# Kernel tuning notes

Hardware: AMD Instinct MI355X
Metric: run time of the kernel (lower is better)

The kernel has to match this reference:

```python
import jax, jax.numpy as jnp
import numpy as np

N_NODES = 100000
N_EDGES = 1000000
EMB_DIM = 64
N_LAYERS = 5
NUM_CLASS = 10
NUM_GRAPHS = 128
BN_EPS = 1e-5


def setup_inputs() -> dict:
    key = jax.random.key(0)
    ks = jax.random.split(key, 16)
    s = 0.05
    inp = {
        "x": jnp.zeros((N_NODES,), dtype=jnp.int64),
        "edge_index": jax.random.randint(ks[0], (2, N_EDGES), 0, N_NODES, dtype=jnp.int64),
        "edge_attr": jax.random.normal(ks[1], (N_EDGES, 7), dtype=jnp.float32),
        "batch": jnp.sort(jax.random.randint(ks[2], (N_NODES,), 0, NUM_GRAPHS, dtype=jnp.int64)),
        # parameters
        "node_table": jax.random.normal(ks[3], (1, EMB_DIM), dtype=jnp.float32) * s,
        "ew": jax.random.normal(ks[4], (N_LAYERS, 7, EMB_DIM), dtype=jnp.float32) * s,   # edge_encoder weight
        "eb": jax.random.normal(ks[5], (N_LAYERS, EMB_DIM), dtype=jnp.float32) * s,
        "w1": jax.random.normal(ks[6], (N_LAYERS, EMB_DIM, EMB_DIM), dtype=jnp.float32) * s,
        "b1": jax.random.normal(ks[7], (N_LAYERS, EMB_DIM), dtype=jnp.float32) * s,
        "w2": jax.random.normal(ks[8], (N_LAYERS, EMB_DIM, EMB_DIM), dtype=jnp.float32) * s,
        "b2": jax.random.normal(ks[9], (N_LAYERS, EMB_DIM), dtype=jnp.float32) * s,
        "gamma": jnp.ones((N_LAYERS, EMB_DIM), dtype=jnp.float32),
        "beta": jnp.zeros((N_LAYERS, EMB_DIM), dtype=jnp.float32),
        "pw": jax.random.normal(ks[10], (EMB_DIM, NUM_CLASS), dtype=jnp.float32) * s,
        "pb": jnp.zeros((NUM_CLASS,), dtype=jnp.float32),
    }
    return inp


def reference(x, edge_index, edge_attr, batch, node_table, ew, eb, w1, b1, w2, b2, gamma, beta, pw, pb):
    n = x.shape[0]
    src, dst = edge_index[0], edge_index[1]
    h = node_table[x]  # [N, D] node embedding lookup (all index 0)
    for l in range(N_LAYERS):
        edge_emb = edge_attr @ ew[l] + eb[l]                      # [E, D]
        msg = jax.nn.relu(h[src] + edge_emb)                      # gather + add + relu
        agg = jax.ops.segment_sum(msg, dst, num_segments=n)       # scatter-add
        z = h + agg                                               # (1 + eps)*x with eps=0
        z = jax.nn.relu(z @ w1[l] + b1[l]) @ w2[l] + b2[l]        # GIN MLP
        mu = z.mean(axis=0)
        var = z.var(axis=0)                                       # biased var, matches BN training
        z = (z - mu) * jax.lax.rsqrt(var + BN_EPS) * gamma[l] + beta[l]
        if l != N_LAYERS - 1:
            z = jax.nn.relu(z)                                    # dropout is identity (eval)
        h = z
    # global mean pool over graphs
    sums = jax.ops.segment_sum(h, batch, num_segments=NUM_GRAPHS)           # [B, D]
    cnt = jax.ops.segment_sum(jnp.ones((n,), h.dtype), batch, num_segments=NUM_GRAPHS)
    h_graph = sums / jnp.maximum(cnt, 1.0)[:, None]
    return h_graph @ pw + pb
```

## Files before the change

### kernel.cpp

```cpp
#include <hip/hip_runtime.h>


__global__ void hist_k(const int* __restrict__ dst, int* __restrict__ cnt, int E) {
  int stride = gridDim.x * blockDim.x;
  for (int i = blockIdx.x * blockDim.x + threadIdx.x; i < E; i += stride)
    atomicAdd(&cnt[dst[i]], 1);
}

__global__ void scan_a_k(const int* __restrict__ deg, int* __restrict__ rowptr,
                         int* __restrict__ bsum, int n) {
  __shared__ int s[256];
  int i = blockIdx.x * 256 + threadIdx.x;
  int v = (i < n) ? deg[i] : 0;
  s[threadIdx.x] = v;
  __syncthreads();
  for (int off = 1; off < 256; off <<= 1) {
    int t = (threadIdx.x >= off) ? s[threadIdx.x - off] : 0;
    __syncthreads();
    s[threadIdx.x] += t;
    __syncthreads();
  }
  if (i < n) rowptr[i] = s[threadIdx.x] - v;
  if (threadIdx.x == 255) bsum[blockIdx.x] = s[255];
}

__global__ void scan_b_k(int* __restrict__ bsum, int nb) {
  __shared__ int s[512];
  int t = threadIdx.x;
  int v = (t < nb) ? bsum[t] : 0;
  s[t] = v;
  __syncthreads();
  for (int off = 1; off < 512; off <<= 1) {
    int u = (t >= off) ? s[t - off] : 0;
    __syncthreads();
    s[t] += u;
    __syncthreads();
  }
  if (t < nb) bsum[t] = s[t] - v;
}

__global__ void scan_c_k(int* __restrict__ rowptr, int* __restrict__ cur,
                         const int* __restrict__ bsum, int n, int E) {
  int i = blockIdx.x * 256 + threadIdx.x;
  if (i < n) {
    int r = rowptr[i] + bsum[blockIdx.x];
    rowptr[i] = r;
    cur[i] = r;
  }
  if (i == 0) rowptr[n] = E;
}

__global__ void scatter_k(const int* __restrict__ src, const int* __restrict__ dst,
                          int* __restrict__ cur, float* __restrict__ sea,
                          const float* __restrict__ ea, int E) {
  int stride = gridDim.x * blockDim.x;
  for (int i = blockIdx.x * blockDim.x + threadIdx.x; i < E; i += stride) {
    int d = dst[i];
    int pos = atomicAdd(&cur[d], 1);
    const float* a = ea + (size_t)i * 7;
    float4 lo = make_float4(a[0], a[1], a[2], a[3]);
    float4 hi = make_float4(a[4], a[5], a[6], __int_as_float(src[i]));
    float4* o = (float4*)(sea + (size_t)pos * 8);
    o[0] = lo;
    o[1] = hi;
  }
}

#define NPW 8
template<int MODE>
__global__ __launch_bounds__(256)
void agg_k(const float* __restrict__ hprev, const int* __restrict__ x,
           const float* __restrict__ ntab, const int* __restrict__ rowptr,
           const float* __restrict__ sea, const float* __restrict__ ewl,
           const float* __restrict__ ebl, const float* __restrict__ statsP,
           const float* __restrict__ gamP, const float* __restrict__ betP,
           float* __restrict__ zout, int n) {
  int wv = (blockIdx.x * blockDim.x + threadIdx.x) >> 6;
  int lane = threadIdx.x & 63;
  int g0 = wv * NPW;
  if (g0 >= n) return;
  int gend = g0 + NPW; if (gend > n) gend = n;

  float ew_[7];
#pragma unroll
  for (int k = 0; k < 7; k++) ew_[k] = ewl[k * 64 + lane];
  float ebv = ebl[lane];

  float cnst = 0.f, sc = 1.f, sh = 0.f;
  if (MODE == 0) cnst = ntab[lane];
  if (MODE == 2) {
    float s1 = statsP[lane], s2 = statsP[64 + lane];
    float mu = s1 / (float)n;
    float var = s2 / (float)n - mu * mu;
    sc = gamP[lane] * rsqrtf(var + 1e-5f);
    sh = betP[lane] - mu * sc;
  }

  auto Hg = [&](int row) -> float {
    if (MODE == 1) {
      int xv = __builtin_amdgcn_readfirstlane(x[row]);
      return ntab[(size_t)xv * 64 + lane];
    } else {
      float v = hprev[(size_t)row * 64 + lane];
      return fmaxf(fmaf(v, sc, sh), 0.f);
    }
  };

  int pcur = __builtin_amdgcn_readfirstlane(rowptr[g0]);
  for (int nd = g0; nd < gend; nd++) {
    int pnext = __builtin_amdgcn_readfirstlane(rowptr[nd + 1]);
    float acc = (MODE == 0) ? cnst : Hg(nd);
    int p = pcur;
    for (; p + 4 <= pnext; p += 4) {
      const float* R0 = sea + (size_t)p * 8;
      const float* R1 = R0 + 8;
      const float* R2 = R0 + 16;
      const float* R3 = R0 + 24;
      float h0, h1, h2, h3;
      if (MODE != 0) {
        int s0 = __builtin_amdgcn_readfirstlane(__float_as_int(R0[7]));
        int s1 = __builtin_amdgcn_readfirstlane(__float_as_int(R1[7]));
        int s2 = __builtin_amdgcn_readfirstlane(__float_as_int(R2[7]));
        int s3 = __builtin_amdgcn_readfirstlane(__float_as_int(R3[7]));
        h0 = Hg(s0); h1 = Hg(s1); h2 = Hg(s2); h3 = Hg(s3);
      } else {
        h0 = h1 = h2 = h3 = cnst;
      }
      float m0 = ebv, m1 = ebv, m2 = ebv, m3 = ebv;
#pragma unroll
      for (int k = 0; k < 7; k++) {
        m0 = fmaf(R0[k], ew_[k], m0);
        m1 = fmaf(R1[k], ew_[k], m1);
        m2 = fmaf(R2[k], ew_[k], m2);
        m3 = fmaf(R3[k], ew_[k], m3);
      }
      acc += fmaxf(h0 + m0, 0.f);
      acc += fmaxf(h1 + m1, 0.f);
      acc += fmaxf(h2 + m2, 0.f);
      acc += fmaxf(h3 + m3, 0.f);
    }
    for (; p < pnext; p++) {
      const float* R0 = sea + (size_t)p * 8;
      float h0 = cnst;
      if (MODE != 0) {
        int s0 = __builtin_amdgcn_readfirstlane(__float_as_int(R0[7]));
        h0 = Hg(s0);
      }
      float m0 = ebv;
#pragma unroll
      for (int k = 0; k < 7; k++) m0 = fmaf(R0[k], ew_[k], m0);
      acc += fmaxf(h0 + m0, 0.f);
    }
    zout[(size_t)nd * 64 + lane] = acc;
    pcur = pnext;
  }
}

#define ASTR 132
__global__ __launch_bounds__(256, 3)
void mlp_k(const float* __restrict__ zin, const float* __restrict__ w1l,
           const float* __restrict__ b1l, const float* __restrict__ w2l,
           const float* __restrict__ b2l, float* __restrict__ zout,
           float* __restrict__ statslot, int n) {
  __shared__ float As[64 * ASTR];
  __shared__ float Ws[4096];
  __shared__ float red[128];
  int tid = threadIdx.x;
  int tx = tid & 15, ty = tid >> 4;
  if (tid < 128) red[tid] = 0.f;
  int r0 = blockIdx.x * 128;

  float4 w2r[4];
  {
    const float4* wb = (const float4*)w2l;
#pragma unroll
    for (int it = 0; it < 4; it++) w2r[it] = wb[it * 256 + tid];
  }

  {
    const float4* gz = (const float4*)(zin + (size_t)r0 * 64);
#pragma unroll
    for (int it = 0; it < 8; it++) {
      int f4 = it * 256 + tid;
      int row = f4 >> 4, kq = f4 & 15;
      float4 v = make_float4(0.f, 0.f, 0.f, 0.f);
      if (r0 + row < n) v = gz[f4];
      As[(4 * kq + 0) * ASTR + row] = v.x;
      As[(4 * kq + 1) * ASTR + row] = v.y;
      As[(4 * kq + 2) * ASTR + row] = v.z;
      As[(4 * kq + 3) * ASTR + row] = v.w;
    }
    const float4* wa = (const float4*)w1l;
    float4* wd = (float4*)Ws;
#pragma unroll
    for (int it = 0; it < 4; it++) wd[it * 256 + tid] = wa[it * 256 + tid];
  }
  __syncthreads();

  const float4 b1v = *(const float4*)(b1l + tx * 4);
  float t[8][4];
#pragma unroll
  for (int rr = 0; rr < 8; rr++) {
    t[rr][0] = b1v.x; t[rr][1] = b1v.y; t[rr][2] = b1v.z; t[rr][3] = b1v.w;
  }
#pragma unroll 8
  for (int k = 0; k < 64; k++) {
    float4 aA = *(const float4*)&As[k * ASTR + ty * 8];
    float4 aB = *(const float4*)&As[k * ASTR + ty * 8 + 4];
    float4 b = *(const float4*)&Ws[k * 64 + tx * 4];
    float a[8] = {aA.x, aA.y, aA.z, aA.w, aB.x, aB.y, aB.z, aB.w};
#pragma unroll
    for (int rr = 0; rr < 8; rr++) {
      t[rr][0] = fmaf(a[rr], b.x, t[rr][0]);
      t[rr][1] = fmaf(a[rr], b.y, t[rr][1]);
      t[rr][2] = fmaf(a[rr], b.z, t[rr][2]);
      t[rr][3] = fmaf(a[rr], b.w, t[rr][3]);
    }
  }
  __syncthreads();

#pragma unroll
  for (int cc = 0; cc < 4; cc++)
#pragma unroll
    for (int rr = 0; rr < 8; rr++)
      As[(tx * 4 + cc) * ASTR + ty * 8 + rr] = fmaxf(t[rr][cc], 0.f);
  {
    float4* wd = (float4*)Ws;
#pragma unroll
    for (int it = 0; it < 4; it++) wd[it * 256 + tid] = w2r[it];
  }
  __syncthreads();

  const float4 b2v = *(const float4*)(b2l + tx * 4);
  float o[8][4];
#pragma unroll
  for (int rr = 0; rr < 8; rr++) {
    o[rr][0] = b2v.x; o[rr][1] = b2v.y; o[rr][2] = b2v.z; o[rr][3] = b2v.w;
  }
#pragma unroll 8
  for (int k = 0; k < 64; k++) {
    float4 aA = *(const float4*)&As[k * ASTR + ty * 8];
    float4 aB = *(const float4*)&As[k * ASTR + ty * 8 + 4];
    float4 b = *(const float4*)&Ws[k * 64 + tx * 4];
    float a[8] = {aA.x, aA.y, aA.z, aA.w, aB.x, aB.y, aB.z, aB.w};
#pragma unroll
    for (int rr = 0; rr < 8; rr++) {
      o[rr][0] = fmaf(a[rr], b.x, o[rr][0]);
      o[rr][1] = fmaf(a[rr], b.y, o[rr][1]);
      o[rr][2] = fmaf(a[rr], b.z, o[rr][2]);
      o[rr][3] = fmaf(a[rr], b.w, o[rr][3]);
    }
  }

  float s1[4] = {0.f, 0.f, 0.f, 0.f}, s2[4] = {0.f, 0.f, 0.f, 0.f};
#pragma unroll
  for (int rr = 0; rr < 8; rr++) {
    int grow = r0 + ty * 8 + rr;
    if (grow < n) {
      float4 v = make_float4(o[rr][0], o[rr][1], o[rr][2], o[rr][3]);
      *(float4*)(zout + (size_t)grow * 64 + tx * 4) = v;
#pragma unroll
      for (int cc = 0; cc < 4; cc++) {
        s1[cc] += o[rr][cc];
        s2[cc] = fmaf(o[rr][cc], o[rr][cc], s2[cc]);
      }
    }
  }
#pragma unroll
  for (int cc = 0; cc < 4; cc++) {
    s1[cc] += __shfl_xor(s1[cc], 16); s1[cc] += __shfl_xor(s1[cc], 32);
    s2[cc] += __shfl_xor(s2[cc], 16); s2[cc] += __shfl_xor(s2[cc], 32);
  }
  if ((tid & 48) == 0) {
#pragma unroll
    for (int cc = 0; cc < 4; cc++) {
      atomicAdd(&red[tx * 4 + cc], s1[cc]);
      atomicAdd(&red[64 + tx * 4 + cc], s2[cc]);
    }
  }
  __syncthreads();
  if (tid < 128) atomicAdd(&statslot[tid], red[tid]);
}

__global__ void pool_k(const float* __restrict__ z2, const float* __restrict__ stats,
                       const float* __restrict__ gam, const float* __restrict__ bet,
                       const int* __restrict__ batch, float* __restrict__ gsum,
                       float* __restrict__ gcnt, int n, int ch) {
  int wid = (blockIdx.x * blockDim.x + threadIdx.x) >> 6;
  int lane = threadIdx.x & 63;
  int v0 = wid * ch;
  if (v0 >= n) return;
  int v1 = v0 + ch; if (v1 > n) v1 = n;
  float st1 = stats[lane], st2 = stats[64 + lane];
  float mu = st1 / (float)n;
  float var = st2 / (float)n - mu * mu;
  float sc = gam[lane] * rsqrtf(var + 1e-5f);
  float sh = bet[lane] - mu * sc;
  int curb = batch[v0];
  float acc = 0.f;
  int cnt = 0;
  for (int v = v0; v < v1; v++) {
    int b = batch[v];
    if (b != curb) {
      atomicAdd(&gsum[curb * 64 + lane], acc);
      if (lane == 0) atomicAdd(&gcnt[curb], (float)cnt);
      acc = 0.f; cnt = 0; curb = b;
    }
    acc += fmaf(z2[(size_t)v * 64 + lane], sc, sh);
    cnt++;
  }
  atomicAdd(&gsum[curb * 64 + lane], acc);
  if (lane == 0) atomicAdd(&gcnt[curb], (float)cnt);
}

__global__ void head_k(const float* __restrict__ gsum, const float* __restrict__ gcnt,
                       const float* __restrict__ pw, const float* __restrict__ pb,
                       float* __restrict__ out, int B, int C) {
  for (int idx = threadIdx.x; idx < B * C; idx += blockDim.x) {
    int g = idx / C, c = idx % C;
    float inv = 1.f / fmaxf(gcnt[g], 1.f);
    float s = pb[c];
    for (int d = 0; d < 64; d++)
      s = fmaf(gsum[g * 64 + d] * inv, pw[d * C + c], s);
    out[idx] = s;
  }
}

extern "C" void kernel_launch(void* const* d_in, const int* in_sizes, int n_in,
                              void* d_out, int out_size, void* d_ws, size_t ws_size,
                              hipStream_t stream) {
  const int*   x     = (const int*)d_in[0];
  const int*   ei    = (const int*)d_in[1];
  const float* ea    = (const float*)d_in[2];
  const int*   batch = (const int*)d_in[3];
  const float* ntab  = (const float*)d_in[4];
  const float* ew    = (const float*)d_in[5];
  const float* eb    = (const float*)d_in[6];
  const float* w1    = (const float*)d_in[7];
  const float* b1    = (const float*)d_in[8];
  const float* w2    = (const float*)d_in[9];
  const float* b2    = (const float*)d_in[10];
  const float* gamma = (const float*)d_in[11];
  const float* beta  = (const float*)d_in[12];
  const float* pw    = (const float*)d_in[13];
  const float* pb    = (const float*)d_in[14];
  float* out = (float*)d_out;

  int N = in_sizes[0];
  int E = in_sizes[1] / 2;
  int L = in_sizes[6] / 64;
  int C = in_sizes[14];
  int B = out_size / C;
  bool tab1 = (in_sizes[4] == 64);

  const int* src = ei;
  const int* dst = ei + E;

  char* ws = (char*)d_ws;
  auto alloc = [&](size_t bytes) -> char* {
    char* p = ws;
    ws += (bytes + 255) & ~(size_t)255;
    return p;
  };
  float* hbuf    = (float*)alloc((size_t)N * 64 * 4);
  float* tbuf    = (float*)alloc((size_t)N * 64 * 4);
  int*   rowptr  = (int*)alloc((size_t)(N + 1) * 4);
  int*   cur     = (int*)alloc((size_t)N * 4);
  float* sea     = (float*)alloc((size_t)(E + 8) * 8 * 4);
  int*   bsum    = (int*)alloc(512 * 4);
  float* bnstats = (float*)alloc((size_t)L * 128 * 4);
  float* gsum    = (float*)alloc((size_t)B * 64 * 4);
  float* gcnt    = (float*)alloc((size_t)B * 4);

  hipMemsetAsync(cur, 0, (size_t)N * 4, stream);
  hipMemsetAsync(bnstats, 0, (size_t)L * 128 * 4, stream);
  hipMemsetAsync(gsum, 0, (size_t)B * 64 * 4, stream);
  hipMemsetAsync(gcnt, 0, (size_t)B * 4, stream);

  hist_k<<<2048, 256, 0, stream>>>(dst, cur, E);
  int NB = (N + 255) / 256;
  scan_a_k<<<NB, 256, 0, stream>>>(cur, rowptr, bsum, N);
  scan_b_k<<<1, 512, 0, stream>>>(bsum, NB);
  scan_c_k<<<NB, 256, 0, stream>>>(rowptr, cur, bsum, N, E);
  scatter_k<<<4096, 256, 0, stream>>>(src, dst, cur, sea, ea, E);

  int aggWaves = (N + NPW - 1) / NPW;
  int aggBlocks = (aggWaves * 64 + 255) / 256;
  int mlpBlocks = (N + 127) / 128;
  for (int l = 0; l < L; l++) {
    const float* ewl = ew + (size_t)l * 448;
    const float* ebl = eb + (size_t)l * 64;
    const float* stP = bnstats + (size_t)(l > 0 ? l - 1 : 0) * 128;
    const float* gmP = gamma + (size_t)(l > 0 ? l - 1 : 0) * 64;
    const float* btP = beta + (size_t)(l > 0 ? l - 1 : 0) * 64;
    if (l == 0) {
      if (tab1)
        agg_k<0><<<aggBlocks, 256, 0, stream>>>(hbuf, x, ntab, rowptr, sea, ewl,
                                                ebl, stP, gmP, btP, tbuf, N);
      else
        agg_k<1><<<aggBlocks, 256, 0, stream>>>(hbuf, x, ntab, rowptr, sea, ewl,
                                                ebl, stP, gmP, btP, tbuf, N);
    } else {
      agg_k<2><<<aggBlocks, 256, 0, stream>>>(hbuf, x, ntab, rowptr, sea, ewl,
                                              ebl, stP, gmP, btP, tbuf, N);
    }
    mlp_k<<<mlpBlocks, 256, 0, stream>>>(tbuf, w1 + (size_t)l * 4096,
                                         b1 + (size_t)l * 64,
                                         w2 + (size_t)l * 4096,
                                         b2 + (size_t)l * 64,
                                         hbuf, bnstats + (size_t)l * 128, N);
  }

  int ch = 128;
  int poolWaves = (N + ch - 1) / ch;
  int poolBlocks = (poolWaves + 3) / 4;
  pool_k<<<poolBlocks, 256, 0, stream>>>(hbuf,
                                         bnstats + (size_t)(L - 1) * 128,
                                         gamma + (size_t)(L - 1) * 64,
                                         beta + (size_t)(L - 1) * 64,
                                         batch, gsum, gcnt, N, ch);
  head_k<<<1, 256, 0, stream>>>(gsum, gcnt, pw, pb, out, B, C);
}
```

Before: 675.8 us.

## Flatten per-wave edge loop into 8-wide batches spanning node boundaries

The aggregation kernel now walks each wave's whole edge range as one flat stream in batches of 8 edges. All gathers and edge-feature loads for a batch are issued before node boundaries are resolved, so the per-node 4-wide loop and its scalar remainder loop go away. This is meant to raise memory-level parallelism and avoid short tails on low-degree nodes. The cost is more registers per lane and a divergent-free but branchy boundary-handling loop inside the batch. Separately, the pooling chunk size is halved and the edge buffer padding is enlarged.

After: 637.3 us. 5.7% less time.

```diff
diff --git a/kernel.cpp b/kernel.cpp
--- a/kernel.cpp
+++ b/kernel.cpp
@@ -96,63 +96,67 @@
     sh = betP[lane] - mu * sc;
   }
 
-  auto Hg = [&](int row) -> float {
+  auto raw_ld = [&](int row) -> float {
+    if (MODE == 0) return 0.f;
     if (MODE == 1) {
       int xv = __builtin_amdgcn_readfirstlane(x[row]);
       return ntab[(size_t)xv * 64 + lane];
-    } else {
-      float v = hprev[(size_t)row * 64 + lane];
-      return fmaxf(fmaf(v, sc, sh), 0.f);
-    }
+    }
+    return hprev[(size_t)row * 64 + lane];
   };
-
-  int pcur = __builtin_amdgcn_readfirstlane(rowptr[g0]);
-  for (int nd = g0; nd < gend; nd++) {
-    int pnext = __builtin_amdgcn_readfirstlane(rowptr[nd + 1]);
-    float acc = (MODE == 0) ? cnst : Hg(nd);
-    int p = pcur;
-    for (; p + 4 <= pnext; p += 4) {
-      const float* R0 = sea + (size_t)p * 8;
-      const float* R1 = R0 + 8;
-      const float* R2 = R0 + 16;
-      const float* R3 = R0 + 24;
-      float h0, h1, h2, h3;
-      if (MODE != 0) {
-        int s0 = __builtin_amdgcn_readfirstlane(__float_as_int(R0[7]));
-        int s1 = __builtin_amdgcn_readfirstlane(__float_as_int(R1[7]));
-        int s2 = __builtin_amdgcn_readfirstlane(__float_as_int(R2[7]));
-        int s3 = __builtin_amdgcn_readfirstlane(__float_as_int(R3[7]));
-        h0 = Hg(s0); h1 = Hg(s1); h2 = Hg(s2); h3 = Hg(s3);
-      } else {
-        h0 = h1 = h2 = h3 = cnst;
+  auto finish_h = [&](float v) -> float {
+    if (MODE == 0) return cnst;
+    if (MODE == 1) return v;
+    return fmaxf(fmaf(v, sc, sh), 0.f);
+  };
+
+  int P1 = __builtin_amdgcn_readfirstlane(rowptr[gend]);
+  int p0 = __builtin_amdgcn_readfirstlane(rowptr[g0]);
+  int nd = g0;
+  int pn = __builtin_amdgcn_readfirstlane(rowptr[nd + 1]);
+  float selfv = raw_ld(nd);
+  float acc = 0.f;
+
+  for (int p = p0; p < P1; p += 8) {
+    const float* R[8];
+    int s[8];
+#pragma unroll
+    for (int u = 0; u < 8; u++) {
+      int t = p + u;
+      int q = t < P1 ? t : P1 - 1;
+      R[u] = sea + (size_t)q * 8;
+      s[u] = __builtin_amdgcn_readfirstlane(__float_as_int(R[u][7]));
+    }
+    float h[8];
+#pragma unroll
+    for (int u = 0; u < 8; u++) h[u] = (MODE == 0) ? cnst : raw_ld(s[u]);
+    float m[8];
+#pragma unroll
+    for (int u = 0; u < 8; u++) m[u] = ebv;
+#pragma unroll
+    for (int k = 0; k < 7; k++) {
+#pragma unroll
+      for (int u = 0; u < 8; u++) m[u] = fmaf(R[u][k], ew_[k], m[u]);
+    }
+#pragma unroll
+    for (int u = 0; u < 8; u++) {
+      if (p + u < P1) {
+        while (p + u >= pn) {
+          zout[(size_t)nd * 64 + lane] = finish_h(selfv) + acc;
+          nd++;
+          selfv = raw_ld(nd);
+          pn = __builtin_amdgcn_readfirstlane(rowptr[nd + 1]);
+          acc = 0.f;
+        }
+        acc += fmaxf(finish_h(h[u]) + m[u], 0.f);
       }
-      float m0 = ebv, m1 = ebv, m2 = ebv, m3 = ebv;
-#pragma unroll
-      for (int k = 0; k < 7; k++) {
-        m0 = fmaf(R0[k], ew_[k], m0);
-        m1 = fmaf(R1[k], ew_[k], m1);
-        m2 = fmaf(R2[k], ew_[k], m2);
-        m3 = fmaf(R3[k], ew_[k], m3);
-      }
-      acc += fmaxf(h0 + m0, 0.f);
-      acc += fmaxf(h1 + m1, 0.f);
-      acc += fmaxf(h2 + m2, 0.f);
-      acc += fmaxf(h3 + m3, 0.f);
-    }
-    for (; p < pnext; p++) {
-      const float* R0 = sea + (size_t)p * 8;
-      float h0 = cnst;
-      if (MODE != 0) {
-        int s0 = __builtin_amdgcn_readfirstlane(__float_as_int(R0[7]));
-        h0 = Hg(s0);
-      }
-      float m0 = ebv;
-#pragma unroll
-      for (int k = 0; k < 7; k++) m0 = fmaf(R0[k], ew_[k], m0);
-      acc += fmaxf(h0 + m0, 0.f);
-    }
-    zout[(size_t)nd * 64 + lane] = acc;
-    pcur = pnext;
+    }
+  }
+  while (nd < gend) {
+    zout[(size_t)nd * 64 + lane] = finish_h(selfv) + acc;
+    nd++;
+    acc = 0.f;
+    if (nd < gend) selfv = raw_ld(nd);
   }
 }
 
@@ -366,7 +370,7 @@
   float* tbuf    = (float*)alloc((size_t)N * 64 * 4);
   int*   rowptr  = (int*)alloc((size_t)(N + 1) * 4);
   int*   cur     = (int*)alloc((size_t)N * 4);
-  float* sea     = (float*)alloc((size_t)(E + 8) * 8 * 4);
+  float* sea     = (float*)alloc((size_t)(E + 16) * 8 * 4);
   int*   bsum    = (int*)alloc(512 * 4);
   float* bnstats = (float*)alloc((size_t)L * 128 * 4);
   float* gsum    = (float*)alloc((size_t)B * 64 * 4);
@@ -411,7 +415,7 @@
                                          hbuf, bnstats + (size_t)l * 128, N);
   }
 
-  int ch = 128;
+  int ch = 64;
   int poolWaves = (N + ch - 1) / ch;
   int poolBlocks = (poolWaves + 3) / 4;
   pool_k<<<poolBlocks, 256, 0, stream>>>(hbuf,
```
